# Kernel optimization log

Hardware: AMD Instinct MI355X
Metric: run time of the kernel (lower is better)

Reference implementation:

```python
import jax, jax.numpy as jnp
import numpy as np

NUM_HEAD, D_MODEL, D_K, D_V = 16, 1024, 64, 64
LN_EPS = 1e-6


def setup_inputs() -> dict:
    key = jax.random.key(0)
    ks = jax.random.split(key, 8)
    B, S, Sp = 2, 2048, 2048
    scale = (2.0 / (D_MODEL + D_MODEL)) ** 0.5  # xavier_normal std
    return {
        "query": jax.random.normal(ks[0], (B, S, D_MODEL), jnp.float32),
        "key": jax.random.normal(ks[1], (B, Sp, D_MODEL), jnp.float32),
        "value": jax.random.normal(ks[2], (B, Sp, D_MODEL), jnp.float32),
        "w_q": jax.random.normal(ks[3], (NUM_HEAD * D_K, D_MODEL), jnp.float32) * scale,
        "w_k": jax.random.normal(ks[4], (NUM_HEAD * D_K, D_MODEL), jnp.float32) * scale,
        "w_v": jax.random.normal(ks[5], (NUM_HEAD * D_V, D_MODEL), jnp.float32) * scale,
        "w_o": jax.random.normal(ks[6], (D_MODEL, NUM_HEAD * D_V), jnp.float32) * scale,
        "ln_gamma": jnp.ones((D_MODEL,), jnp.float32),
        "ln_beta": jnp.zeros((D_MODEL,), jnp.float32),
    }


def _layer_norm(x, g, b):
    mu = jnp.mean(x, axis=-1, keepdims=True)
    var = jnp.mean(jnp.square(x - mu), axis=-1, keepdims=True)
    return (x - mu) * jax.lax.rsqrt(var + LN_EPS) * g + b


def reference(query, key, value, w_q, w_k, w_v, w_o, ln_gamma, ln_beta):
    B, S, _ = query.shape
    Sp = key.shape[1]
    residual = query
    qn = _layer_norm(query, ln_gamma, ln_beta)
    # projections: nn.Linear(x) = x @ W.T  (W: [out, in])
    q = (qn @ w_q.T).reshape(B, S, NUM_HEAD, D_K).transpose(0, 2, 1, 3)   # [B,H,S,dk]
    k = (key @ w_k.T).reshape(B, Sp, NUM_HEAD, D_K).transpose(0, 2, 1, 3)  # [B,H,S',dk]
    v = (value @ w_v.T).reshape(B, Sp, NUM_HEAD, D_V).transpose(0, 2, 1, 3)  # [B,H,S',dv]
    scores = jnp.einsum("bhsd,bhtd->bhst", q, k) / (D_K ** 0.5)  # [B,H,S,S']
    attn = jax.nn.softmax(scores, axis=-1)
    out = jnp.einsum("bhst,bhtd->bhsd", attn, v)  # [B,H,S,dv]
    out = out.transpose(0, 2, 1, 3).reshape(B, S, NUM_HEAD * D_V)
    out = out @ w_o.T  # dropout is identity in eval mode
    out = out + residual
    return out, attn


if __name__ == "__main__":
    o, a = reference(**setup_inputs())
    print(o.shape, a.shape)
```

## Files before the change

kernel.cpp:

```cpp
#include <hip/hip_runtime.h>
#include <hip/hip_bf16.h>


typedef __bf16 bf16x8 __attribute__((ext_vector_type(8)));
typedef __bf16 bf16x4 __attribute__((ext_vector_type(4)));
typedef float  f32x4  __attribute__((ext_vector_type(4)));
typedef float  f32x16 __attribute__((ext_vector_type(16)));

#define NUM_HEAD 16
#define SEQ 2048
#define DMODEL 1024
#define DK 64
#define MROWS 4096
#define LOG2E 1.44269504088896340736f

__device__ __forceinline__ void gload_lds16(const void* g, void* l) {
    __builtin_amdgcn_global_load_lds((const __attribute__((address_space(1))) void*)g,
                                     (__attribute__((address_space(3))) void*)l, 16, 0, 0);
}

__global__ __launch_bounds__(256) void ln_cast(const float* __restrict__ x,
                                               const float* __restrict__ g,
                                               const float* __restrict__ bt,
                                               __bf16* __restrict__ y,
                                               const float* __restrict__ key,
                                               const float* __restrict__ value,
                                               const float* __restrict__ wq,
                                               const float* __restrict__ wk,
                                               const float* __restrict__ wv,
                                               const float* __restrict__ wo,
                                               __bf16* kb, __bf16* vb, __bf16* wqb,
                                               __bf16* wkb, __bf16* wvb, __bf16* wob) {
    int tid = threadIdx.x;
    if (blockIdx.x < 4096) {
        int row = blockIdx.x;
        __shared__ float red[2][4];
        float4 v = ((const float4*)(x + (size_t)row * DMODEL))[tid];
        float s  = v.x + v.y + v.z + v.w;
        float sq = v.x * v.x + v.y * v.y + v.z * v.z + v.w * v.w;
        #pragma unroll
        for (int o = 32; o; o >>= 1) { s += __shfl_xor(s, o, 64); sq += __shfl_xor(sq, o, 64); }
        int wv_ = tid >> 6;
        if ((tid & 63) == 0) { red[0][wv_] = s; red[1][wv_] = sq; }
        __syncthreads();
        s  = red[0][0] + red[0][1] + red[0][2] + red[0][3];
        sq = red[1][0] + red[1][1] + red[1][2] + red[1][3];
        float mu  = s * (1.0f / DMODEL);
        float var = sq * (1.0f / DMODEL) - mu * mu;
        float rs  = rsqrtf(var + 1e-6f);
        float4 gg = ((const float4*)g)[tid];
        float4 bb = ((const float4*)bt)[tid];
        bf16x4 o;
        o[0] = (__bf16)((v.x - mu) * rs * gg.x + bb.x);
        o[1] = (__bf16)((v.y - mu) * rs * gg.y + bb.y);
        o[2] = (__bf16)((v.z - mu) * rs * gg.z + bb.z);
        o[3] = (__bf16)((v.w - mu) * rs * gg.w + bb.w);
        *(bf16x4*)&y[(size_t)row * DMODEL + tid * 4] = o;
    } else {
        int i = (blockIdx.x - 4096) * 256 + tid;
        const float* src; __bf16* dst; int off;
        if (i < 1048576)      { src = key;   dst = kb;  off = i; }
        else if (i < 2097152) { src = value; dst = vb;  off = i - 1048576; }
        else if (i < 2359296) { src = wq;    dst = wqb; off = i - 2097152; }
        else if (i < 2621440) { src = wk;    dst = wkb; off = i - 2359296; }
        else if (i < 2883584) { src = wv;    dst = wvb; off = i - 2621440; }
        else                  { src = wo;    dst = wob; off = i - 2883584; }
        float4 v = ((const float4*)src)[off];
        bf16x4 o = {(__bf16)v.x, (__bf16)v.y, (__bf16)v.z, (__bf16)v.w};
        *(bf16x4*)&dst[(size_t)off * 4] = o;
    }
}

__device__ __forceinline__ void gemm_core64(const __bf16* __restrict__ Arow,
                                            const __bf16* __restrict__ Brow,
                                            __bf16 (*As)[64], __bf16 (*Bs)[64],
                                            int tid, int wr, int wc, int lr, int lg,
                                            f32x4 (&acc)[4][2]) {
    for (int kt = 0; kt < 1024; kt += 64) {
        __syncthreads();
        #pragma unroll
        for (int c = 0; c < 4; ++c) {
            int row = c * 32 + (tid >> 3);
            int col = ((tid & 7) ^ (row & 7)) * 8;
            gload_lds16(&Arow[(size_t)row * 1024 + kt + col], &As[row][(tid & 7) * 8]);
        }
        #pragma unroll
        for (int c = 0; c < 2; ++c) {
            int row = c * 32 + (tid >> 3);
            int col = ((tid & 7) ^ (row & 7)) * 8;
            gload_lds16(&Brow[(size_t)row * 1024 + kt + col], &Bs[row][(tid & 7) * 8]);
        }
        __syncthreads();
        #pragma unroll
        for (int kk = 0; kk < 2; ++kk) {
            bf16x8 af[4], bg[2];
            #pragma unroll
            for (int m = 0; m < 4; ++m) {
                int row = wr + m * 16 + lr;
                int slot = (kk * 4 + lg) ^ (row & 7);
                af[m] = *(const bf16x8*)&As[row][slot * 8];
            }
            #pragma unroll
            for (int n = 0; n < 2; ++n) {
                int row = wc + n * 16 + lr;
                int slot = (kk * 4 + lg) ^ (row & 7);
                bg[n] = *(const bf16x8*)&Bs[row][slot * 8];
            }
            #pragma unroll
            for (int m = 0; m < 4; ++m)
                #pragma unroll
                for (int n = 0; n < 2; ++n)
                    acc[m][n] = __builtin_amdgcn_mfma_f32_16x16x32_bf16(af[m], bg[n], acc[m][n], 0, 0, 0);
        }
    }
}

__global__ __launch_bounds__(256) void qkv_proj(const __bf16* __restrict__ qn,
                                                const __bf16* __restrict__ kb,
                                                const __bf16* __restrict__ vb,
                                                const __bf16* __restrict__ wqb,
                                                const __bf16* __restrict__ wkb,
                                                const __bf16* __restrict__ wvb,
                                                __bf16* __restrict__ Qp,
                                                __bf16* __restrict__ Kp,
                                                __bf16* __restrict__ Vt) {
    __shared__ __bf16 As[128][64];
    __shared__ __bf16 Bs[64][64];
    int mode = blockIdx.x >> 9;
    int t = blockIdx.x & 511;
    int tm = t >> 4, tn = t & 15;
    int tid = threadIdx.x, lane = tid & 63, wv = tid >> 6;
    int wr = (wv >> 1) * 64, wc = (wv & 1) * 32;
    int lr = lane & 15, lg = lane >> 4;

    const __bf16* A = (mode == 0) ? qn : (mode == 1) ? kb : vb;
    const __bf16* W = (mode == 0) ? wqb : (mode == 1) ? wkb : wvb;

    f32x4 acc[4][2] = {};
    gemm_core64(A + (size_t)(tm * 128) * 1024, W + (size_t)(tn * 64) * 1024,
                As, Bs, tid, wr, wc, lr, lg, acc);

    if (mode < 2) {
        float scale = (mode == 0) ? (0.125f * LOG2E) : 1.0f;
        __bf16* C = (mode == 0) ? Qp : Kp;
        #pragma unroll
        for (int m = 0; m < 4; ++m)
            #pragma unroll
            for (int n = 0; n < 2; ++n)
                #pragma unroll
                for (int r = 0; r < 4; ++r) {
                    int grow = tm * 128 + wr + m * 16 + lg * 4 + r;
                    int gcol = tn * 64 + wc + n * 16 + lr;
                    int b = grow >> 11, ss = grow & 2047, h = gcol >> 6, d = gcol & 63;
                    C[((size_t)(b * NUM_HEAD + h) * SEQ + ss) * DK + d] = (__bf16)(acc[m][n][r] * scale);
                }
    } else {
        #pragma unroll
        for (int m = 0; m < 4; ++m)
            #pragma unroll
            for (int n = 0; n < 2; ++n)
                #pragma unroll
                for (int r = 0; r < 4; ++r) {
                    int grow = tm * 128 + wr + m * 16 + lg * 4 + r;
                    int gcol = tn * 64 + wc + n * 16 + lr;
                    int b = grow >> 11, ss = grow & 2047, h = gcol >> 6, d = gcol & 63;
                    Vt[((size_t)(b * NUM_HEAD + h) * DK + d) * SEQ + ss] = (__bf16)acc[m][n][r];
                }
    }
}

__global__ __launch_bounds__(256) void out_gemm(const __bf16* __restrict__ A,
                                                const __bf16* __restrict__ Bw,
                                                const float* __restrict__ residual,
                                                float* __restrict__ out) {
    __shared__ __bf16 As[128][64];
    __shared__ __bf16 Bs[64][64];
    int tm = blockIdx.x >> 4, tn = blockIdx.x & 15;
    int tid = threadIdx.x, lane = tid & 63, wv = tid >> 6;
    int wr = (wv >> 1) * 64, wc = (wv & 1) * 32;
    int lr = lane & 15, lg = lane >> 4;

    f32x4 acc[4][2] = {};
    gemm_core64(A + (size_t)(tm * 128) * 1024, Bw + (size_t)(tn * 64) * 1024,
                As, Bs, tid, wr, wc, lr, lg, acc);

    #pragma unroll
    for (int m = 0; m < 4; ++m)
        #pragma unroll
        for (int n = 0; n < 2; ++n)
            #pragma unroll
            for (int r = 0; r < 4; ++r) {
                int grow = tm * 128 + wr + m * 16 + lg * 4 + r;
                int gcol = tn * 64 + wc + n * 16 + lr;
                size_t idx = (size_t)grow * DMODEL + gcol;
                out[idx] = acc[m][n][r] + residual[idx];
            }
}

__global__ __launch_bounds__(256) void attn8(const __bf16* __restrict__ Qp,
                                             const __bf16* __restrict__ Kp,
                                             const __bf16* __restrict__ Vt,
                                             float* __restrict__ attn_out,
                                             __bf16* __restrict__ out_heads) {
    __shared__ __bf16 Ks[2][128][64];
    __shared__ __bf16 Vs[2][64][128];

    int bid = blockIdx.x;
    int wid = (bid & 7) * 64 + (bid >> 3);
    int bh = wid >> 4;
    int qbase = (wid & 15) * 128;
    int tid = threadIdx.x, lane = tid & 63, wv = tid >> 6;
    int l31 = lane & 31, hi = lane >> 5;
    int qw = qbase + wv * 32;

    const __bf16* Qh = Qp + ((size_t)bh * SEQ + qw) * DK;
    const __bf16* Kh = Kp + (size_t)bh * SEQ * DK;
    const __bf16* Vh = Vt + (size_t)bh * DK * SEQ;

    bf16x8 qf[4];
    #pragma unroll
    for (int s = 0; s < 4; ++s)
        qf[s] = *(const bf16x8*)&Qh[(size_t)l31 * DK + s * 16 + hi * 8];

    int krow = tid >> 3, ksc = tid & 7;
    auto stageK = [&](int buf, int kc) {
        #pragma unroll
        for (int j = 0; j < 4; ++j) {
            int row = j * 32 + krow;
            gload_lds16(&Kh[(size_t)(kc + row) * DK + ((ksc ^ (row & 7)) * 8)],
                        &Ks[buf][row][ksc * 8]);
        }
    };
    int vrow16 = tid >> 4, vslot = tid & 15;
    auto stageV = [&](int buf, int kc) {
        #pragma unroll
        for (int j = 0; j < 4; ++j) {
            int row = j * 16 + vrow16;
            gload_lds16(&Vh[(size_t)row * SEQ + kc + ((vslot ^ (row & 7)) * 8)],
                        &Vs[buf][row][vslot * 8]);
        }
    };
    auto readK = [&](int buf, int row, int s) -> bf16x8 {
        int slot = (2 * s + hi) ^ (row & 7);
        return *(const bf16x8*)&Ks[buf][row][slot * 8];
    };
    auto readV = [&](int buf, int drow, int g) -> bf16x8 {
        int slot = g ^ (drow & 7);
        return *(const bf16x8*)&Vs[buf][drow][slot * 8];
    };

    float lsum = 0.f;
    auto tileA = [&](int buf, int toff) {
        bf16x8 kf[4];
        #pragma unroll
        for (int s = 0; s < 4; ++s) kf[s] = readK(buf, toff + l31, s);
        f32x16 dd;
        #pragma unroll
        for (int r = 0; r < 16; ++r) dd[r] = 0.f;
        __builtin_amdgcn_s_setprio(1);
        #pragma unroll
        for (int s = 0; s < 4; ++s)
            dd = __builtin_amdgcn_mfma_f32_32x32x16_bf16(kf[s], qf[s], dd, 0, 0, 0);
        __builtin_amdgcn_s_setprio(0);
        float es[4] = {0.f, 0.f, 0.f, 0.f};
        #pragma unroll
        for (int r = 0; r < 16; ++r) es[r & 3] += exp2f(dd[r]);
        lsum += (es[0] + es[1]) + (es[2] + es[3]);
    };

    stageK(0, 0);
    for (int c = 0; c < 16; ++c) {
        __syncthreads();
        if (c + 1 < 16) stageK((c + 1) & 1, (c + 1) * 128);
        tileA(c & 1, 0);
        tileA(c & 1, 32);
        tileA(c & 1, 64);
        tileA(c & 1, 96);
        __syncthreads();
    }
    lsum += __shfl_xor(lsum, 32, 64);
    float invl = 1.0f / lsum;

    float* attn_base = attn_out + ((size_t)bh * SEQ + qw) * SEQ;
    f32x16 o0, o1;
    #pragma unroll
    for (int r = 0; r < 16; ++r) { o0[r] = 0.f; o1[r] = 0.f; }

    auto tileB = [&](int buf, int kglob, int toff) {
        bf16x8 kf[4];
        #pragma unroll
        for (int s = 0; s < 4; ++s) kf[s] = readK(buf, toff + l31, s);
        f32x16 dd;
        #pragma unroll
        for (int r = 0; r < 16; ++r) dd[r] = 0.f;
        __builtin_amdgcn_s_setprio(1);
        #pragma unroll
        for (int s = 0; s < 4; ++s)
            dd = __builtin_amdgcn_mfma_f32_32x32x16_bf16(kf[s], qf[s], dd, 0, 0, 0);
        __builtin_amdgcn_s_setprio(0);

        int gb = toff >> 3;
        bf16x8 vf00 = readV(buf, l31,      gb + hi);
        bf16x8 vf01 = readV(buf, 32 + l31, gb + hi);
        bf16x8 vf10 = readV(buf, l31,      gb + 2 + hi);
        bf16x8 vf11 = readV(buf, 32 + l31, gb + 2 + hi);

        float p[16];
        #pragma unroll
        for (int r = 0; r < 16; ++r) p[r] = exp2f(dd[r]) * invl;

        int k0 = kglob + toff;
        #pragma unroll
        for (int q4 = 0; q4 < 4; ++q4) {
            f32x4 v4 = {p[4 * q4], p[4 * q4 + 1], p[4 * q4 + 2], p[4 * q4 + 3]};
            *(f32x4*)&attn_base[(size_t)l31 * SEQ + k0 + 8 * q4 + 4 * hi] = v4;
        }

        unsigned int w[8];
        #pragma unroll
        for (int i = 0; i < 8; ++i) {
            union { __bf16 h[2]; unsigned int u; } bw;
            bw.h[0] = (__bf16)p[2 * i];
            bw.h[1] = (__bf16)p[2 * i + 1];
            w[i] = bw.u;
        }
        __builtin_amdgcn_s_setprio(1);
        {
            unsigned int a0 = w[0], a1 = w[1], a2 = w[2], a3 = w[3];
            asm volatile("v_permlane32_swap_b32 %0, %1" : "+v"(a0), "+v"(a2));
            asm volatile("v_permlane32_swap_b32 %0, %1" : "+v"(a1), "+v"(a3));
            union { unsigned int u[4]; bf16x8 v; } pa;
            pa.u[0] = a0; pa.u[1] = a1; pa.u[2] = a2; pa.u[3] = a3;
            o0 = __builtin_amdgcn_mfma_f32_32x32x16_bf16(pa.v, vf00, o0, 0, 0, 0);
            o1 = __builtin_amdgcn_mfma_f32_32x32x16_bf16(pa.v, vf01, o1, 0, 0, 0);
        }
        {
            unsigned int a0 = w[4], a1 = w[5], a2 = w[6], a3 = w[7];
            asm volatile("v_permlane32_swap_b32 %0, %1" : "+v"(a0), "+v"(a2));
            asm volatile("v_permlane32_swap_b32 %0, %1" : "+v"(a1), "+v"(a3));
            union { unsigned int u[4]; bf16x8 v; } pa;
            pa.u[0] = a0; pa.u[1] = a1; pa.u[2] = a2; pa.u[3] = a3;
            o0 = __builtin_amdgcn_mfma_f32_32x32x16_bf16(pa.v, vf10, o0, 0, 0, 0);
            o1 = __builtin_amdgcn_mfma_f32_32x32x16_bf16(pa.v, vf11, o1, 0, 0, 0);
        }
        __builtin_amdgcn_s_setprio(0);
    };

    stageK(0, 0);
    stageV(0, 0);
    for (int c = 0; c < 16; ++c) {
        __syncthreads();
        if (c + 1 < 16) { stageK((c + 1) & 1, (c + 1) * 128); stageV((c + 1) & 1, (c + 1) * 128); }
        tileB(c & 1, c * 128, 0);
        tileB(c & 1, c * 128, 32);
        tileB(c & 1, c * 128, 64);
        tileB(c & 1, c * 128, 96);
        __syncthreads();
    }

    int b = bh >> 4, h = bh & 15;
    #pragma unroll
    for (int r = 0; r < 16; ++r) {
        int q = (r & 3) + 8 * (r >> 2) + 4 * hi;
        __bf16* orow = &out_heads[((size_t)(b * SEQ + qw + q)) * DMODEL + h * DK];
        orow[l31]      = (__bf16)o0[r];
        orow[32 + l31] = (__bf16)o1[r];
    }
}

extern "C" void kernel_launch(void* const* d_in, const int* in_sizes, int n_in,
                              void* d_out, int out_size, void* d_ws, size_t ws_size,
                              hipStream_t stream) {
    const float* query = (const float*)d_in[0];
    const float* key   = (const float*)d_in[1];
    const float* value = (const float*)d_in[2];
    const float* w_q   = (const float*)d_in[3];
    const float* w_k   = (const float*)d_in[4];
    const float* w_v   = (const float*)d_in[5];
    const float* w_o   = (const float*)d_in[6];
    const float* lng   = (const float*)d_in[7];
    const float* lnb   = (const float*)d_in[8];

    char* ws = (char*)d_ws;
    __bf16* qn  = (__bf16*)(ws);
    __bf16* kb  = (__bf16*)(ws + ( 8u << 20));
    __bf16* vb  = (__bf16*)(ws + (16u << 20));
    __bf16* wqb = (__bf16*)(ws + (24u << 20));
    __bf16* wkb = (__bf16*)(ws + (26u << 20));
    __bf16* wvb = (__bf16*)(ws + (28u << 20));
    __bf16* wob = (__bf16*)(ws + (30u << 20));
    __bf16* Qp  = (__bf16*)(ws + (32u << 20));
    __bf16* Kp  = (__bf16*)(ws + (40u << 20));
    __bf16* Vt  = (__bf16*)(ws + (48u << 20));
    __bf16* oh  = (__bf16*)(ws + (56u << 20));

    float* out  = (float*)d_out;
    float* attn = out + (size_t)MROWS * DMODEL;

    ln_cast<<<16384, 256, 0, stream>>>(query, lng, lnb, qn,
                                       key, value, w_q, w_k, w_v, w_o,
                                       kb, vb, wqb, wkb, wvb, wob);

    qkv_proj<<<1536, 256, 0, stream>>>(qn, kb, vb, wqb, wkb, wvb, Qp, Kp, Vt);

    attn8<<<512, 256, 0, stream>>>(Qp, Kp, Vt, attn, oh);

    out_gemm<<<512, 256, 0, stream>>>(oh, wob, query, out);
}
```

Before: 270.7 us.

## Split softmax row-sum pass into separate kernel with key-split parallelism

```diff
diff --git a/kernel.cpp b/kernel.cpp
--- a/kernel.cpp
+++ b/kernel.cpp
@@ -197,9 +197,71 @@
             }
 }
 
+__global__ __launch_bounds__(256) void attn_lsum(const __bf16* __restrict__ Qp,
+                                                 const __bf16* __restrict__ Kp,
+                                                 float* __restrict__ invlrow) {
+    __shared__ float lred[4][32];
+
+    int bid = blockIdx.x;
+    int wid = (bid & 7) * 256 + (bid >> 3);
+    int bh = wid >> 6;
+    int qbase = (wid & 63) * 32;
+    int tid = threadIdx.x, lane = tid & 63, wv = tid >> 6;
+    int l31 = lane & 31, hi = lane >> 5;
+
+    const __bf16* Qh = Qp + ((size_t)bh * SEQ + qbase) * DK;
+    const __bf16* Kh = Kp + (size_t)bh * SEQ * DK;
+
+    bf16x8 qf[4];
+    #pragma unroll
+    for (int s = 0; s < 4; ++s)
+        qf[s] = *(const bf16x8*)&Qh[(size_t)l31 * DK + s * 16 + hi * 8];
+
+    int kbase = wv * 512;
+    auto loadK = [&](bf16x8 (&kf)[4], int k0) {
+        #pragma unroll
+        for (int s = 0; s < 4; ++s)
+            kf[s] = *(const bf16x8*)&Kh[(size_t)(k0 + l31) * DK + s * 16 + hi * 8];
+    };
+
+    float lsum = 0.f;
+    auto tileA = [&](const bf16x8 (&kf)[4]) {
+        f32x16 dd;
+        #pragma unroll
+        for (int r = 0; r < 16; ++r) dd[r] = 0.f;
+        __builtin_amdgcn_s_setprio(1);
+        #pragma unroll
+        for (int s = 0; s < 4; ++s)
+            dd = __builtin_amdgcn_mfma_f32_32x32x16_bf16(kf[s], qf[s], dd, 0, 0, 0);
+        __builtin_amdgcn_s_setprio(0);
+        float es[4] = {0.f, 0.f, 0.f, 0.f};
+        #pragma unroll
+        for (int r = 0; r < 16; ++r) es[r & 3] += exp2f(dd[r]);
+        lsum += (es[0] + es[1]) + (es[2] + es[3]);
+    };
+    {
+        bf16x8 kA[4], kB[4];
+        loadK(kA, kbase);
+        for (int t = 0; t < 16; t += 2) {
+            loadK(kB, kbase + (t + 1) * 32);
+            tileA(kA);
+            if (t + 2 < 16) loadK(kA, kbase + (t + 2) * 32);
+            tileA(kB);
+        }
+    }
+    lsum += __shfl_xor(lsum, 32, 64);
+    if (hi == 0) lred[wv][l31] = lsum;
+    __syncthreads();
+    if (tid < 32) {
+        float l = lred[0][tid] + lred[1][tid] + lred[2][tid] + lred[3][tid];
+        invlrow[(size_t)bh * SEQ + qbase + tid] = 1.0f / l;
+    }
+}
+
 __global__ __launch_bounds__(256) void attn8(const __bf16* __restrict__ Qp,
                                              const __bf16* __restrict__ Kp,
                                              const __bf16* __restrict__ Vt,
+                                             const float* __restrict__ invlrow,
                                              float* __restrict__ attn_out,
                                              __bf16* __restrict__ out_heads) {
     __shared__ __bf16 Ks[2][128][64];
@@ -222,6 +284,8 @@
     for (int s = 0; s < 4; ++s)
         qf[s] = *(const bf16x8*)&Qh[(size_t)l31 * DK + s * 16 + hi * 8];
 
+    float invl = invlrow[(size_t)bh * SEQ + qw + l31];
+
     int krow = tid >> 3, ksc = tid & 7;
     auto stageK = [&](int buf, int kc) {
         #pragma unroll
@@ -248,38 +312,6 @@
         int slot = g ^ (drow & 7);
         return *(const bf16x8*)&Vs[buf][drow][slot * 8];
     };
-
-    float lsum = 0.f;
-    auto tileA = [&](int buf, int toff) {
-        bf16x8 kf[4];
-        #pragma unroll
-        for (int s = 0; s < 4; ++s) kf[s] = readK(buf, toff + l31, s);
-        f32x16 dd;
-        #pragma unroll
-        for (int r = 0; r < 16; ++r) dd[r] = 0.f;
-        __builtin_amdgcn_s_setprio(1);
-        #pragma unroll
-        for (int s = 0; s < 4; ++s)
-            dd = __builtin_amdgcn_mfma_f32_32x32x16_bf16(kf[s], qf[s], dd, 0, 0, 0);
-        __builtin_amdgcn_s_setprio(0);
-        float es[4] = {0.f, 0.f, 0.f, 0.f};
-        #pragma unroll
-        for (int r = 0; r < 16; ++r) es[r & 3] += exp2f(dd[r]);
-        lsum += (es[0] + es[1]) + (es[2] + es[3]);
-    };
-
-    stageK(0, 0);
-    for (int c = 0; c < 16; ++c) {
-        __syncthreads();
-        if (c + 1 < 16) stageK((c + 1) & 1, (c + 1) * 128);
-        tileA(c & 1, 0);
-        tileA(c & 1, 32);
-        tileA(c & 1, 64);
-        tileA(c & 1, 96);
-        __syncthreads();
-    }
-    lsum += __shfl_xor(lsum, 32, 64);
-    float invl = 1.0f / lsum;
 
     float* attn_base = attn_out + ((size_t)bh * SEQ + qw) * SEQ;
     f32x16 o0, o1;
@@ -393,6 +425,7 @@
     __bf16* Kp  = (__bf16*)(ws + (40u << 20));
     __bf16* Vt  = (__bf16*)(ws + (48u << 20));
     __bf16* oh  = (__bf16*)(ws + (56u << 20));
+    float*  l2i = (float*)(ws + (64u << 20));
 
     float* out  = (float*)d_out;
     float* attn = out + (size_t)MROWS * DMODEL;
@@ -403,7 +436,8 @@
 
     qkv_proj<<<1536, 256, 0, stream>>>(qn, kb, vb, wqb, wkb, wvb, Qp, Kp, Vt);
 
-    attn8<<<512, 256, 0, stream>>>(Qp, Kp, Vt, attn, oh);
+    attn_lsum<<<2048, 256, 0, stream>>>(Qp, Kp, l2i);
+    attn8<<<512, 256, 0, stream>>>(Qp, Kp, Vt, l2i, attn, oh);
 
     out_gemm<<<512, 256, 0, stream>>>(oh, wob, query, out);
 }
```

Measured after the change: 297.5 us. 1.1x slower.
